# Kernel tuning notes

Hardware: AMD Instinct MI355X
Metric: run time of the kernel (lower is better)

Reference implementation:

```python
import jax, jax.numpy as jnp
import numpy as np

ALPHA = 0.5  # mixing weight between dot-product and wedge-norm terms


def setup_inputs() -> dict:
    key = jax.random.key(0)
    kq, kk, kv = jax.random.split(key, 3)
    B, L, H, E = 2, 2048, 8, 32
    queries = jax.random.normal(kq, (B, L, H, E), dtype=jnp.float32)
    keys = jax.random.normal(kk, (B, L, H, E), dtype=jnp.float32)
    values = jax.random.normal(kv, (B, L, H, E), dtype=jnp.float32)
    return {"queries": queries, "keys": keys, "values": values}


def reference(queries, keys, values):
    # queries: [B,L,H,E], keys: [B,S,H,E], values: [B,S,H,D]
    E = queries.shape[-1]
    scale = 1.0 / jnp.sqrt(jnp.asarray(E, dtype=queries.dtype))
    # dot product scores: [B,H,L,S]
    dot = jnp.einsum('blhe,bshe->bhls', queries, keys)
    # squared norms -> broadcastable [B,H,L,1] and [B,H,1,S]
    qn2 = jnp.sum(queries ** 2, axis=-1).transpose(0, 2, 1)[..., :, None]
    kn2 = jnp.sum(keys ** 2, axis=-1).transpose(0, 2, 1)[..., None, :]
    # wedge (Clifford) squared norm, clamped at 0
    wedge = jax.nn.relu(qn2 * kn2 - dot ** 2)
    scores = (ALPHA * dot - (1.0 - ALPHA) * wedge) * scale
    attn = jax.nn.softmax(scores, axis=-1)  # [B,H,L,S]
    # out: [B,L,H,D]
    out = jnp.einsum('bhls,bshd->blhd', attn, values)
    return out
```

## Files before the change

### kernel.cpp

```cpp
#include <hip/hip_runtime.h>
#include <hip/hip_bf16.h>
#include <math.h>


#define NB 2
#define NL 2048
#define NS 2048
#define NH 8
#define NBH 16
#define STRIPS 4
#define NT 16
#define CSC 0.12751742f
#define DEFER_THR 24.0f

#define WS_KN2_OFF 0u
#define WS_KHKL_OFF 131072u
#define WS_VT_OFF (131072u + 4194304u)
#define WS_PACC_OFF (131072u + 4194304u + 2097152u)
#define WS_PML_OFF (WS_PACC_OFF + 16777216u)
#define WS_NEED (WS_PML_OFF + 1048576u)

typedef float f32x4 __attribute__((ext_vector_type(4)));
typedef float f32x2 __attribute__((ext_vector_type(2)));
typedef short s16x8 __attribute__((ext_vector_type(8)));
typedef unsigned short u16;

__device__ inline unsigned pk2(float a, float b) {
    __hip_bfloat162 t = __float22bfloat162_rn(make_float2(a, b));
    union { __hip_bfloat162 h; unsigned u; } cv;
    cv.h = t;
    return cv.u;
}
template <int CTRL>
__device__ inline float dpp_add(float x) {
    return x + __int_as_float(__builtin_amdgcn_mov_dpp(__float_as_int(x), CTRL, 0xF, 0xF, false));
}
__device__ inline void dma16(const void* gp, void* lp) {
    __builtin_amdgcn_global_load_lds(
        (__attribute__((address_space(1))) void*)(void*)gp,
        (__attribute__((address_space(3))) void*)lp, 16, 0, 0);
}
__device__ inline void pl32(unsigned& a, unsigned& b) {
    asm("v_permlane32_swap_b32 %0, %1" : "+v"(a), "+v"(b));
}
__device__ inline void pl16(unsigned& a, unsigned& b) {
    asm("v_permlane16_swap_b32 %0, %1" : "+v"(a), "+v"(b));
}
__device__ inline int swzK(int row) { return (row ^ (row >> 2)) & 3; }
__device__ inline int swzV(int row) { return (row + (row >> 3)) & 7; }

__global__ __launch_bounds__(256) void ga_pre(const float* __restrict__ K,
                                              const float* __restrict__ V,
                                              float* __restrict__ kn2w,
                                              u16* __restrict__ khkl,
                                              u16* __restrict__ vtw) {
    __shared__ float Vf[64][36];
    const int T = threadIdx.x;
    const int bh = blockIdx.x >> 5, stile = blockIdx.x & 31;
    const int b = bh >> 3, h = bh & 7;
    const int s0 = stile * 64;
    const int sk = T >> 2, kc = T & 3;

    const float* kp = K + ((size_t)((b * NS + s0 + sk) * NH + h)) * 32 + kc * 8;
    float4 f0 = *(const float4*)kp, f1 = *(const float4*)(kp + 4);
    float kx[8] = {f0.x, f0.y, f0.z, f0.w, f1.x, f1.y, f1.z, f1.w};
    unsigned hh[4], ll[4];
    float kn2p = 0.f;
#pragma unroll
    for (int i = 0; i < 4; i++) {
        float x0 = kx[2 * i], x1 = kx[2 * i + 1];
        kn2p = fmaf(x0, x0, kn2p);
        kn2p = fmaf(x1, x1, kn2p);
        unsigned h01 = pk2(x0, x1);
        hh[i] = h01;
        float h0 = __uint_as_float(h01 << 16);
        float h1 = __uint_as_float(h01 & 0xffff0000u);
        ll[i] = pk2(x0 - h0, x1 - h1);
    }
    u16* kd = khkl + ((size_t)(bh * NS + s0 + sk)) * 64;
    const int swk = sk & 7;
    *(uint4*)(kd + ((kc ^ swk) * 8)) = make_uint4(hh[0], hh[1], hh[2], hh[3]);
    *(uint4*)(kd + (((4 + kc) ^ swk) * 8)) = make_uint4(ll[0], ll[1], ll[2], ll[3]);
    kn2p = dpp_add<0xB1>(kn2p);
    kn2p = dpp_add<0x4E>(kn2p);
    if (kc == 0) kn2w[bh * NS + s0 + sk] = kn2p;

    const float* vp = V + ((size_t)((b * NS + s0 + sk) * NH + h)) * 32 + kc * 8;
    float4 g0 = *(const float4*)vp, g1 = *(const float4*)(vp + 4);
    const int chv = kc ^ ((sk >> 3) & 3);
    *(float4*)&Vf[sk][chv * 8] = g0;
    *(float4*)&Vf[sk][chv * 8 + 4] = g1;
    __syncthreads();
    const int dr = T >> 3, c = T & 7;
    float vv[8];
#pragma unroll
    for (int i = 0; i < 8; i++)
        vv[i] = Vf[c * 8 + i][(((dr >> 3) ^ (c & 3)) << 3) + (dr & 7)];
    *(uint4*)(vtw + ((size_t)(bh * 32 + dr)) * NS + s0 + c * 8) =
        make_uint4(pk2(vv[0], vv[1]), pk2(vv[2], vv[3]), pk2(vv[4], vv[5]), pk2(vv[6], vv[7]));
}

__global__ __launch_bounds__(256, 3) void ga_wave(
    const float* __restrict__ Q, const float* __restrict__ kn2w,
    const u16* __restrict__ khkl, const u16* __restrict__ vtw,
    float* __restrict__ pacc, float* __restrict__ pml) {
    __shared__ u16 sK[4][2][32][64];
    __shared__ u16 sV[4][2][32][32];

    const int T = threadIdx.x;
    const int lane = T & 63, wave = T >> 6;
    const int g = lane >> 4, lc = lane & 15, g8 = g * 8;
    const int blk = blockIdx.x;
    const int qt = blk & 15, strip = (blk >> 4) & 3, bh = blk >> 6;
    const int b = bh >> 3, h = bh & 7;
    const int qwa = qt * 128 + wave * 16;
    const int qwb = qwa + 64;
    const int kb0 = strip * 512;

    s16x8 qha, qla, qhb, qlb;
    float qn2a, qn2b;
    {
        const float* qrow = Q + ((size_t)((b * NL + qwa + lc) * NH + h)) * 32 + g8;
        float4 qa = *(const float4*)qrow, qb = *(const float4*)(qrow + 4);
        float q8[8] = {qa.x, qa.y, qa.z, qa.w, qb.x, qb.y, qb.z, qb.w};
        union { unsigned u4[4]; s16x8 v; } qh_, ql_;
        float qn2 = 0.f;
#pragma unroll
        for (int i = 0; i < 4; i++) {
            float x0 = q8[2 * i], x1 = q8[2 * i + 1];
            qn2 = fmaf(x0, x0, qn2);
            qn2 = fmaf(x1, x1, qn2);
            unsigned h01 = pk2(x0, x1);
            qh_.u4[i] = h01;
            float h0 = __uint_as_float(h01 << 16);
            float h1 = __uint_as_float(h01 & 0xffff0000u);
            ql_.u4[i] = pk2(x0 - h0, x1 - h1);
        }
        qha = qh_.v; qla = ql_.v;
        qn2 += __shfl_xor(qn2, 16);
        qn2 += __shfl_xor(qn2, 32);
        qn2a = qn2;
    }
    {
        const float* qrow = Q + ((size_t)((b * NL + qwb + lc) * NH + h)) * 32 + g8;
        float4 qa = *(const float4*)qrow, qb = *(const float4*)(qrow + 4);
        float q8[8] = {qa.x, qa.y, qa.z, qa.w, qb.x, qb.y, qb.z, qb.w};
        union { unsigned u4[4]; s16x8 v; } qh_, ql_;
        float qn2 = 0.f;
#pragma unroll
        for (int i = 0; i < 4; i++) {
            float x0 = q8[2 * i], x1 = q8[2 * i + 1];
            qn2 = fmaf(x0, x0, qn2);
            qn2 = fmaf(x1, x1, qn2);
            unsigned h01 = pk2(x0, x1);
            qh_.u4[i] = h01;
            float h0 = __uint_as_float(h01 << 16);
            float h1 = __uint_as_float(h01 & 0xffff0000u);
            ql_.u4[i] = pk2(x0 - h0, x1 - h1);
        }
        qhb = qh_.v; qlb = ql_.v;
        qn2 += __shfl_xor(qn2, 16);
        qn2 += __shfl_xor(qn2, 32);
        qn2b = qn2;
    }

    const char* ksrc = (const char*)khkl + (size_t)(bh * NS + kb0) * 128 + lane * 16;
    const char* vsrc = (const char*)vtw +
        ((size_t)(bh * 32 + (lane >> 2)) * NS + kb0 + (lane & 3) * 8) * 2;
    const float* kn2b = kn2w + (size_t)bh * NS + kb0 + 4 * g;

    u16(*mK)[32][64] = sK[wave];
    u16(*mV)[32][32] = sV[wave];

    {
        dma16(ksrc, &mK[0][0][0]);
        dma16(ksrc + 1024, &mK[0][8][0]);
        dma16(ksrc + 2048, &mK[0][16][0]);
        dma16(ksrc + 3072, &mK[0][24][0]);
        dma16(vsrc, &mV[0][0][0]);
        dma16(vsrc + 16 * NS * 2, &mV[0][16][0]);
    }

    s16x8 ones;
#pragma unroll
    for (int i = 0; i < 8; i++) ones[i] = (short)0x3F80;

    f32x4 acc0a = {0.f, 0.f, 0.f, 0.f}, acc1a = {0.f, 0.f, 0.f, 0.f};
    f32x4 acc0b = {0.f, 0.f, 0.f, 0.f}, acc1b = {0.f, 0.f, 0.f, 0.f};
    f32x4 lacca = {0.f, 0.f, 0.f, 0.f}, laccb = {0.f, 0.f, 0.f, 0.f};
    float ma = -1e30f, mb = -1e30f;
    const f32x4 z = {0.f, 0.f, 0.f, 0.f};
    const int sw = lc & 7;

#pragma unroll 1
    for (int t = 0; t < NT; ++t) {
        asm volatile("s_waitcnt lgkmcnt(0)" ::: "memory");
        f32x4 kn20 = *(const f32x4*)(kn2b + t * 32);
        f32x4 kn21 = *(const f32x4*)(kn2b + t * 32 + 16);
        __builtin_amdgcn_sched_barrier(0);
        if (t + 1 < NT) {
            const char* k2 = ksrc + (size_t)(t + 1) * 4096;
            const char* v2 = vsrc + (size_t)(t + 1) * 64;
            const int nb = (t + 1) & 1;
            dma16(k2, &mK[nb][0][0]);
            dma16(k2 + 1024, &mK[nb][8][0]);
            dma16(k2 + 2048, &mK[nb][16][0]);
            dma16(k2 + 3072, &mK[nb][24][0]);
            dma16(v2, &mV[nb][0][0]);
            dma16(v2 + 16 * NS * 2, &mV[nb][16][0]);
            asm volatile("s_waitcnt vmcnt(6)" ::: "memory");
        } else {
            asm volatile("s_waitcnt vmcnt(0)" ::: "memory");
        }
        __builtin_amdgcn_sched_barrier(0);

        const int buf = t & 1;
        s16x8 kh0 = *(s16x8*)&mK[buf][lc][(g ^ sw) * 8];
        s16x8 kl0 = *(s16x8*)&mK[buf][lc][((4 + g) ^ sw) * 8];
        s16x8 kh1 = *(s16x8*)&mK[buf][16 + lc][(g ^ sw) * 8];
        s16x8 kl1 = *(s16x8*)&mK[buf][16 + lc][((4 + g) ^ sw) * 8];
        f32x4 da0, da1, db0, db1;
        {
            f32x4 dd = __builtin_amdgcn_mfma_f32_16x16x32_bf16(kl0, qha, z, 0, 0, 0);
            dd = __builtin_amdgcn_mfma_f32_16x16x32_bf16(kh0, qla, dd, 0, 0, 0);
            da0 = __builtin_amdgcn_mfma_f32_16x16x32_bf16(kh0, qha, dd, 0, 0, 0);
            dd = __builtin_amdgcn_mfma_f32_16x16x32_bf16(kl1, qha, z, 0, 0, 0);
            dd = __builtin_amdgcn_mfma_f32_16x16x32_bf16(kh1, qla, dd, 0, 0, 0);
            da1 = __builtin_amdgcn_mfma_f32_16x16x32_bf16(kh1, qha, dd, 0, 0, 0);
            dd = __builtin_amdgcn_mfma_f32_16x16x32_bf16(kl0, qhb, z, 0, 0, 0);
            dd = __builtin_amdgcn_mfma_f32_16x16x32_bf16(kh0, qlb, dd, 0, 0, 0);
            db0 = __builtin_amdgcn_mfma_f32_16x16x32_bf16(kh0, qhb, dd, 0, 0, 0);
            dd = __builtin_amdgcn_mfma_f32_16x16x32_bf16(kl1, qhb, z, 0, 0, 0);
            dd = __builtin_amdgcn_mfma_f32_16x16x32_bf16(kh1, qlb, dd, 0, 0, 0);
            db1 = __builtin_amdgcn_mfma_f32_16x16x32_bf16(kh1, qhb, dd, 0, 0, 0);
        }
        s16x8 vlo = *(s16x8*)&mV[buf][lc][g8];
        s16x8 vhi = *(s16x8*)&mV[buf][16 + lc][g8];

        float sca[2][4], scb[2][4];
        {
            const f32x2 qa2 = {qn2a, qn2a}, qb2 = {qn2b, qn2b};
            f32x4 kn2m[2] = {kn20, kn21};
            f32x4 dam[2] = {da0, da1}, dbm[2] = {db0, db1};
#pragma unroll
            for (int st = 0; st < 2; st++) {
                f32x2 kk0 = {kn2m[st][0], kn2m[st][1]}, kk1 = {kn2m[st][2], kn2m[st][3]};
                f32x2 dd0 = {dam[st][0], dam[st][1]}, dd1 = {dam[st][2], dam[st][3]};
                f32x2 e0 = dd0 - qa2 * kk0;
                f32x2 e1 = dd1 - qa2 * kk1;
                f32x2 t0 = dd0 * dd0 + e0;
                f32x2 t1 = dd1 * dd1 + e1;
                sca[st][0] = fminf(dam[st][0], t0[0]);
                sca[st][1] = fminf(dam[st][1], t0[1]);
                sca[st][2] = fminf(dam[st][2], t1[0]);
                sca[st][3] = fminf(dam[st][3], t1[1]);
                f32x2 ee0 = {dbm[st][0], dbm[st][1]}, ee1 = {dbm[st][2], dbm[st][3]};
                f32x2 f0 = ee0 - qb2 * kk0;
                f32x2 f1 = ee1 - qb2 * kk1;
                f32x2 u0 = ee0 * ee0 + f0;
                f32x2 u1 = ee1 * ee1 + f1;
                scb[st][0] = fminf(dbm[st][0], u0[0]);
                scb[st][1] = fminf(dbm[st][1], u0[1]);
                scb[st][2] = fminf(dbm[st][2], u1[0]);
                scb[st][3] = fminf(dbm[st][3], u1[1]);
            }
        }

        float tma = fmaxf(fmaxf(fmaxf(sca[0][0], sca[0][1]), fmaxf(sca[0][2], sca[0][3])),
                          fmaxf(fmaxf(sca[1][0], sca[1][1]), fmaxf(sca[1][2], sca[1][3])));
        float tmb = fmaxf(fmaxf(fmaxf(scb[0][0], scb[0][1]), fmaxf(scb[0][2], scb[0][3])),
                          fmaxf(fmaxf(scb[1][0], scb[1][1]), fmaxf(scb[1][2], scb[1][3])));
        if (!__all((tma <= ma + DEFER_THR) && (tmb <= mb + DEFER_THR))) {
            tma = fmaxf(tma, __shfl_xor(tma, 16));
            tma = fmaxf(tma, __shfl_xor(tma, 32));
            tmb = fmaxf(tmb, __shfl_xor(tmb, 16));
            tmb = fmaxf(tmb, __shfl_xor(tmb, 32));
            const float nma = fmaxf(ma, tma), nmb = fmaxf(mb, tmb);
            const float ala = __builtin_amdgcn_exp2f((ma - nma) * CSC);
            const float alb = __builtin_amdgcn_exp2f((mb - nmb) * CSC);
            ma = nma; mb = nmb;
            acc0a *= ala; acc1a *= ala; lacca *= ala;
            acc0b *= alb; acc1b *= alb; laccb *= alb;
        }
        const float negmaC = -ma * CSC, negmbC = -mb * CSC;
        const f32x2 cscv = {CSC, CSC};
        const f32x2 nmav = {negmaC, negmaC}, nmbv = {negmbC, negmbC};
        float pa[2][4], pb[2][4];
#pragma unroll
        for (int st = 0; st < 2; st++) {
            f32x2 s0 = {sca[st][0], sca[st][1]}, s1 = {sca[st][2], sca[st][3]};
            f32x2 e0 = s0 * cscv + nmav;
            f32x2 e1 = s1 * cscv + nmav;
            pa[st][0] = __builtin_amdgcn_exp2f(e0[0]);
            pa[st][1] = __builtin_amdgcn_exp2f(e0[1]);
            pa[st][2] = __builtin_amdgcn_exp2f(e1[0]);
            pa[st][3] = __builtin_amdgcn_exp2f(e1[1]);
            f32x2 u0 = {scb[st][0], scb[st][1]}, u1 = {scb[st][2], scb[st][3]};
            f32x2 f0 = u0 * cscv + nmbv;
            f32x2 f1 = u1 * cscv + nmbv;
            pb[st][0] = __builtin_amdgcn_exp2f(f0[0]);
            pb[st][1] = __builtin_amdgcn_exp2f(f0[1]);
            pb[st][2] = __builtin_amdgcn_exp2f(f1[0]);
            pb[st][3] = __builtin_amdgcn_exp2f(f1[1]);
        }

        {
            unsigned w00 = pk2(pa[0][0], pa[0][1]), w01 = pk2(pa[0][2], pa[0][3]);
            unsigned w10 = pk2(pa[1][0], pa[1][1]), w11 = pk2(pa[1][2], pa[1][3]);
            pl32(w00, w10); pl32(w01, w11);
            pl16(w00, w10); pl16(w01, w11);
            union { uint4 u; s16x8 v; } P;
            P.u = make_uint4(w00, w01, w10, w11);
            acc0a = __builtin_amdgcn_mfma_f32_16x16x32_bf16(vlo, P.v, acc0a, 0, 0, 0);
            acc1a = __builtin_amdgcn_mfma_f32_16x16x32_bf16(vhi, P.v, acc1a, 0, 0, 0);
            lacca = __builtin_amdgcn_mfma_f32_16x16x32_bf16(ones, P.v, lacca, 0, 0, 0);
        }
        {
            unsigned w00 = pk2(pb[0][0], pb[0][1]), w01 = pk2(pb[0][2], pb[0][3]);
            unsigned w10 = pk2(pb[1][0], pb[1][1]), w11 = pk2(pb[1][2], pb[1][3]);
            pl32(w00, w10); pl32(w01, w11);
            pl16(w00, w10); pl16(w01, w11);
            union { uint4 u; s16x8 v; } P;
            P.u = make_uint4(w00, w01, w10, w11);
            acc0b = __builtin_amdgcn_mfma_f32_16x16x32_bf16(vlo, P.v, acc0b, 0, 0, 0);
            acc1b = __builtin_amdgcn_mfma_f32_16x16x32_bf16(vhi, P.v, acc1b, 0, 0, 0);
            laccb = __builtin_amdgcn_mfma_f32_16x16x32_bf16(ones, P.v, laccb, 0, 0, 0);
        }
    }

    float* paa = pacc + (((size_t)bh * STRIPS + strip) * NL + (qwa + lc)) * 32;
    *(f32x4*)(paa + 4 * g) = acc0a;
    *(f32x4*)(paa + 16 + 4 * g) = acc1a;
    float* pab = pacc + (((size_t)bh * STRIPS + strip) * NL + (qwb + lc)) * 32;
    *(f32x4*)(pab + 4 * g) = acc0b;
    *(f32x4*)(pab + 16 + 4 * g) = acc1b;
    if (g == 0) {
        *(float2*)(pml + (((size_t)bh * STRIPS + strip) * NL + (qwa + lc)) * 2) =
            make_float2(ma, lacca[0]);
        *(float2*)(pml + (((size_t)bh * STRIPS + strip) * NL + (qwb + lc)) * 2) =
            make_float2(mb, laccb[0]);
    }
}

__global__ __launch_bounds__(256) void ga_combine(const float* __restrict__ pacc,
                                                  const float* __restrict__ pml,
                                                  float* __restrict__ O) {
    const int tid = blockIdx.x * 256 + threadIdx.x;
    const int dq = tid & 7, q = (tid >> 3) & 2047, bh = tid >> 14;
    const int b = bh >> 3, h = bh & 7;
    float m[4], l[4];
#pragma unroll
    for (int s = 0; s < 4; s++) {
        float2 t = *(const float2*)(pml + (((size_t)bh * STRIPS + s) * NL + q) * 2);
        m[s] = t.x;
        l[s] = t.y;
    }
    float mf = fmaxf(fmaxf(m[0], m[1]), fmaxf(m[2], m[3]));
    float w[4], L = 0.f;
#pragma unroll
    for (int s = 0; s < 4; s++) {
        w[s] = __builtin_amdgcn_exp2f((m[s] - mf) * CSC);
        L = fmaf(l[s], w[s], L);
    }
    const float inv = 1.f / L;
    float4 o = make_float4(0.f, 0.f, 0.f, 0.f);
#pragma unroll
    for (int s = 0; s < 4; s++) {
        const float* pa = pacc + (((size_t)bh * STRIPS + s) * NL + q) * 32 + dq * 4;
        float4 a = *(const float4*)pa;
        o.x = fmaf(a.x, w[s], o.x);
        o.y = fmaf(a.y, w[s], o.y);
        o.z = fmaf(a.z, w[s], o.z);
        o.w = fmaf(a.w, w[s], o.w);
    }
    o.x *= inv; o.y *= inv; o.z *= inv; o.w *= inv;
    *(float4*)(O + (((size_t)(b * NL + q)) * NH + h) * 32 + dq * 4) = o;
}

__global__ __launch_bounds__(512, 4) void ga_fallback(
    const float* __restrict__ Q, const float* __restrict__ K,
    const float* __restrict__ V, float* __restrict__ O) {
    __shared__ union {
        struct {
            u16 Kh[2][64][32];
            u16 Kl[2][64][32];
            u16 Vt[2][32][64];
            float kn2[2][64];
        } s;
        struct { float acc[8][32][17]; float m[8][16]; float l[8][16]; } c;
    } u;
    __shared__ u16 sP[8][16][64];

    const int T = threadIdx.x;
    const int lane = T & 63, wave = T >> 6;
    const int g = lane >> 4, lc = lane & 15, g8 = g * 8;
    const int half = wave >> 2;
    const int qt = blockIdx.x & 31;
    const int bh = blockIdx.x >> 5;
    const int b = bh >> 3, h = bh & 7;
    const int qw = qt * 64 + (wave & 3) * 16;

    const float* qrow = Q + ((size_t)((b * NL + qw + lc) * NH + h)) * 32 + g8;
    float4 qa = *(const float4*)qrow, qb = *(const float4*)(qrow + 4);
    float q8[8] = {qa.x, qa.y, qa.z, qa.w, qb.x, qb.y, qb.z, qb.w};
    union { unsigned u4[4]; s16x8 v; } qh_, ql_;
    float qn2 = 0.f;
#pragma unroll
    for (int i = 0; i < 4; i++) {
        float x0 = q8[2 * i], x1 = q8[2 * i + 1];
        qn2 = fmaf(x0, x0, qn2);
        qn2 = fmaf(x1, x1, qn2);
        unsigned h01 = pk2(x0, x1);
        qh_.u4[i] = h01;
        float h0 = __uint_as_float(h01 << 16);
        float h1 = __uint_as_float(h01 & 0xffff0000u);
        ql_.u4[i] = pk2(x0 - h0, x1 - h1);
    }
    const s16x8 qh = qh_.v, ql = ql_.v;
    qn2 += __shfl_xor(qn2, 16);
    qn2 += __shfl_xor(qn2, 32);

    const int Tl = T & 255;
    const int sk = Tl >> 2, kc = Tl & 3;
    const int dv = Tl & 31, vc = Tl >> 5;
    const float* kbase = K + ((size_t)(b * NS * NH) + h) * 32;
    const float* vbase = V + ((size_t)(b * NS * NH) + h) * 32;
    const int kphys = (kc ^ swzK(sk)) * 8;
    const int vphys = (vc ^ swzV(dv)) * 8;

    int s0 = half * 1024;
    float4 ka = *(const float4*)(kbase + (size_t)(s0 + sk) * 256 + kc * 8);
    float4 kb = *(const float4*)(kbase + (size_t)(s0 + sk) * 256 + kc * 8 + 4);
    float vr[8];
#pragma unroll
    for (int i = 0; i < 8; i++) vr[i] = vbase[(size_t)(s0 + 8 * vc + i) * 256 + dv];

    f32x4 acc0 = {0.f, 0.f, 0.f, 0.f}, acc1 = {0.f, 0.f, 0.f, 0.f};
    float m = -INFINITY, l = 0.f;

    for (int t = 0; t < 16; ++t) {
        {
            float kx[8] = {ka.x, ka.y, ka.z, ka.w, kb.x, kb.y, kb.z, kb.w};
            unsigned hh[4], ll[4];
            float kn2p = 0.f;
#pragma unroll
            for (int i = 0; i < 4; i++) {
                float x0 = kx[2 * i], x1 = kx[2 * i + 1];
                kn2p = fmaf(x0, x0, kn2p);
                kn2p = fmaf(x1, x1, kn2p);
                unsigned h01 = pk2(x0, x1);
                hh[i] = h01;
                float h0 = __uint_as_float(h01 << 16);
                float h1 = __uint_as_float(h01 & 0xffff0000u);
                ll[i] = pk2(x0 - h0, x1 - h1);
            }
            *(uint4*)&u.s.Kh[half][sk][kphys] = make_uint4(hh[0], hh[1], hh[2], hh[3]);
            *(uint4*)&u.s.Kl[half][sk][kphys] = make_uint4(ll[0], ll[1], ll[2], ll[3]);
            kn2p = dpp_add<0xB1>(kn2p);
            kn2p = dpp_add<0x4E>(kn2p);
            if (kc == 0) u.s.kn2[half][sk] = kn2p;
            *(uint4*)&u.s.Vt[half][dv][vphys] =
                make_uint4(pk2(vr[0], vr[1]), pk2(vr[2], vr[3]),
                           pk2(vr[4], vr[5]), pk2(vr[6], vr[7]));
        }
        const int tn = (t + 1 < 16) ? t + 1 : t;
        const int sn = half * 1024 + tn * 64;
        ka = *(const float4*)(kbase + (size_t)(sn + sk) * 256 + kc * 8);
        kb = *(const float4*)(kbase + (size_t)(sn + sk) * 256 + kc * 8 + 4);
#pragma unroll
        for (int i = 0; i < 8; i++) vr[i] = vbase[(size_t)(sn + 8 * vc + i) * 256 + dv];

        __syncthreads();

        f32x4 d[4], kn2v[4];
        const f32x4 z = {0.f, 0.f, 0.f, 0.f};
        const int skr = swzK(lc);
#pragma unroll
        for (int st = 0; st < 4; st++) {
            kn2v[st] = *(f32x4*)&u.s.kn2[half][16 * st + 4 * g];
            s16x8 kh = *(s16x8*)&u.s.Kh[half][16 * st + lc][(g ^ skr) * 8];
            s16x8 kl = *(s16x8*)&u.s.Kl[half][16 * st + lc][(g ^ skr) * 8];
            f32x4 dd = __builtin_amdgcn_mfma_f32_16x16x32_bf16(kl, qh, z, 0, 0, 0);
            dd = __builtin_amdgcn_mfma_f32_16x16x32_bf16(kh, ql, dd, 0, 0, 0);
            dd = __builtin_amdgcn_mfma_f32_16x16x32_bf16(kh, qh, dd, 0, 0, 0);
            d[st] = dd;
        }

        float sc[4][4];
#pragma unroll
        for (int st = 0; st < 4; st++)
#pragma unroll
            for (int r = 0; r < 4; r++) {
                float dd = d[st][r];
                float w = fmaxf(fmaf(-dd, dd, qn2 * kn2v[st][r]), 0.f);
                sc[st][r] = (dd - w) * CSC;
            }

        float x0 = fmaxf(fmaxf(sc[0][0], sc[0][1]), fmaxf(sc[0][2], sc[0][3]));
        float x1 = fmaxf(fmaxf(sc[1][0], sc[1][1]), fmaxf(sc[1][2], sc[1][3]));
        float x2 = fmaxf(fmaxf(sc[2][0], sc[2][1]), fmaxf(sc[2][2], sc[2][3]));
        float x3 = fmaxf(fmaxf(sc[3][0], sc[3][1]), fmaxf(sc[3][2], sc[3][3]));
        float tm = fmaxf(fmaxf(x0, x1), fmaxf(x2, x3));
        tm = fmaxf(tm, __shfl_xor(tm, 16));
        tm = fmaxf(tm, __shfl_xor(tm, 32));
        const float nm = fmaxf(m, tm);
        const float al = __builtin_amdgcn_exp2f(m - nm);
        m = nm;
        float p[4][4], ls = 0.f;
#pragma unroll
        for (int st = 0; st < 4; st++)
#pragma unroll
            for (int r = 0; r < 4; r++) {
                p[st][r] = __builtin_amdgcn_exp2f(sc[st][r] - nm);
                ls += p[st][r];
            }
        l = fmaf(l, al, ls);
        acc0 *= al;
        acc1 *= al;

#pragma unroll
        for (int st = 0; st < 4; st++) {
            const int off = ((2 * st + (g >> 1)) ^ (lc & 7)) * 8 + (g & 1) * 4;
            *(uint2*)&sP[wave][lc][off] =
                make_uint2(pk2(p[st][0], p[st][1]), pk2(p[st][2], p[st][3]));
        }
        __builtin_amdgcn_s_waitcnt(0xC07F);

        const int svl = swzV(lc), svh = swzV(lc + 16), spl = lc & 7;
        s16x8 va00 = *(s16x8*)&u.s.Vt[half][lc][(g ^ svl) * 8];
        s16x8 va01 = *(s16x8*)&u.s.Vt[half][lc][((4 + g) ^ svl) * 8];
        s16x8 va10 = *(s16x8*)&u.s.Vt[half][lc + 16][(g ^ svh) * 8];
        s16x8 va11 = *(s16x8*)&u.s.Vt[half][lc + 16][((4 + g) ^ svh) * 8];
        s16x8 pb0 = *(s16x8*)&sP[wave][lc][(g ^ spl) * 8];
        s16x8 pb1 = *(s16x8*)&sP[wave][lc][((4 + g) ^ spl) * 8];
        acc0 = __builtin_amdgcn_mfma_f32_16x16x32_bf16(va00, pb0, acc0, 0, 0, 0);
        acc0 = __builtin_amdgcn_mfma_f32_16x16x32_bf16(va01, pb1, acc0, 0, 0, 0);
        acc1 = __builtin_amdgcn_mfma_f32_16x16x32_bf16(va10, pb0, acc1, 0, 0, 0);
        acc1 = __builtin_amdgcn_mfma_f32_16x16x32_bf16(va11, pb1, acc1, 0, 0, 0);

        __syncthreads();
    }

    l += __shfl_xor(l, 16);
    l += __shfl_xor(l, 32);
#pragma unroll
    for (int r = 0; r < 4; r++) {
        u.c.acc[wave][4 * g + r][lc] = acc0[r];
        u.c.acc[wave][16 + 4 * g + r][lc] = acc1[r];
    }
    if (lane < 16) {
        u.c.m[wave][lc] = m;
        u.c.l[wave][lc] = l;
    }
    __syncthreads();

    const int q = T >> 3, dq = (T & 7) * 4, qr = q & 15;
    const int w0 = q >> 4, w1 = w0 + 4;
    float m0 = u.c.m[w0][qr], m1 = u.c.m[w1][qr];
    float l0 = u.c.l[w0][qr], l1 = u.c.l[w1][qr];
    float mf = fmaxf(m0, m1);
    float e0 = __builtin_amdgcn_exp2f(m0 - mf);
    float e1 = __builtin_amdgcn_exp2f(m1 - mf);
    float inv = 1.f / fmaf(l1, e1, l0 * e0);
    e0 *= inv;
    e1 *= inv;
    float4 o;
    o.x = u.c.acc[w0][dq + 0][qr] * e0 + u.c.acc[w1][dq + 0][qr] * e1;
    o.y = u.c.acc[w0][dq + 1][qr] * e0 + u.c.acc[w1][dq + 1][qr] * e1;
    o.z = u.c.acc[w0][dq + 2][qr] * e0 + u.c.acc[w1][dq + 2][qr] * e1;
    o.w = u.c.acc[w0][dq + 3][qr] * e0 + u.c.acc[w1][dq + 3][qr] * e1;
    *(float4*)(O + ((size_t)((b * NL + qt * 64 + q) * NH + h)) * 32 + dq) = o;
}

extern "C" void kernel_launch(void* const* d_in, const int* in_sizes, int n_in,
                              void* d_out, int out_size, void* d_ws, size_t ws_size,
                              hipStream_t stream) {
    const float* Q = (const float*)d_in[0];
    const float* K = (const float*)d_in[1];
    const float* V = (const float*)d_in[2];
    float* O = (float*)d_out;

    if (ws_size >= (size_t)WS_NEED) {
        float* kn2w = (float*)((char*)d_ws + WS_KN2_OFF);
        u16* khkl = (u16*)((char*)d_ws + WS_KHKL_OFF);
        u16* vtw = (u16*)((char*)d_ws + WS_VT_OFF);
        float* pacc = (float*)((char*)d_ws + WS_PACC_OFF);
        float* pml = (float*)((char*)d_ws + WS_PML_OFF);
        ga_pre<<<NBH * 32, 256, 0, stream>>>(K, V, kn2w, khkl, vtw);
        ga_wave<<<NBH * 16 * STRIPS, 256, 0, stream>>>(Q, kn2w, khkl, vtw, pacc, pml);
        ga_combine<<<(NBH * NL * 8) / 256, 256, 0, stream>>>(pacc, pml, O);
    } else {
        ga_fallback<<<NBH * 32, 512, 0, stream>>>(Q, K, V, O);
    }
}
```

Measured before the change: 106.8 us.

## Replace per-wave LDS DMA staging with register double-buffered global loads

The main attention kernel stops staging K/V tiles through per-wave LDS buffers filled by global_load_lds DMA. Each lane now loads its MFMA operands straight from global memory into registers, double-buffered across two tile sets (A/B) so the next tile's loads overlap the current tile's compute. The K swizzle in the preprocessing kernel is removed to match the direct loads. The block index mapping is also reordered so consecutive blocks share a query tile across (bh, strip) groups. This frees LDS and drops the LDS round-trip, at the cost of more VGPRs and of relying on L2/cache for the reuse of K/V across waves.

```diff
diff --git a/kernel.cpp b/kernel.cpp
--- a/kernel.cpp
+++ b/kernel.cpp
@@ -34,11 +34,6 @@
 template <int CTRL>
 __device__ inline float dpp_add(float x) {
     return x + __int_as_float(__builtin_amdgcn_mov_dpp(__float_as_int(x), CTRL, 0xF, 0xF, false));
-}
-__device__ inline void dma16(const void* gp, void* lp) {
-    __builtin_amdgcn_global_load_lds(
-        (__attribute__((address_space(1))) void*)(void*)gp,
-        (__attribute__((address_space(3))) void*)lp, 16, 0, 0);
 }
 __device__ inline void pl32(unsigned& a, unsigned& b) {
     asm("v_permlane32_swap_b32 %0, %1" : "+v"(a), "+v"(b));
@@ -78,9 +73,8 @@
         ll[i] = pk2(x0 - h0, x1 - h1);
     }
     u16* kd = khkl + ((size_t)(bh * NS + s0 + sk)) * 64;
-    const int swk = sk & 7;
-    *(uint4*)(kd + ((kc ^ swk) * 8)) = make_uint4(hh[0], hh[1], hh[2], hh[3]);
-    *(uint4*)(kd + (((4 + kc) ^ swk) * 8)) = make_uint4(ll[0], ll[1], ll[2], ll[3]);
+    *(uint4*)(kd + kc * 8) = make_uint4(hh[0], hh[1], hh[2], hh[3]);
+    *(uint4*)(kd + (4 + kc) * 8) = make_uint4(ll[0], ll[1], ll[2], ll[3]);
     kn2p = dpp_add<0xB1>(kn2p);
     kn2p = dpp_add<0x4E>(kn2p);
     if (kc == 0) kn2w[bh * NS + s0 + sk] = kn2p;
@@ -100,18 +94,16 @@
         make_uint4(pk2(vv[0], vv[1]), pk2(vv[2], vv[3]), pk2(vv[4], vv[5]), pk2(vv[6], vv[7]));
 }
 
-__global__ __launch_bounds__(256, 3) void ga_wave(
+__global__ __launch_bounds__(256, 3) void ga_rpipe(
     const float* __restrict__ Q, const float* __restrict__ kn2w,
     const u16* __restrict__ khkl, const u16* __restrict__ vtw,
     float* __restrict__ pacc, float* __restrict__ pml) {
-    __shared__ u16 sK[4][2][32][64];
-    __shared__ u16 sV[4][2][32][32];
-
     const int T = threadIdx.x;
     const int lane = T & 63, wave = T >> 6;
     const int g = lane >> 4, lc = lane & 15, g8 = g * 8;
     const int blk = blockIdx.x;
-    const int qt = blk & 15, strip = (blk >> 4) & 3, bh = blk >> 6;
+    const int qt = blk >> 6, grp = blk & 63;
+    const int bh = grp >> 2, strip = grp & 3;
     const int b = bh >> 3, h = bh & 7;
     const int qwa = qt * 128 + wave * 16;
     const int qwb = qwa + 64;
@@ -164,22 +156,9 @@
         qn2b = qn2;
     }
 
-    const char* ksrc = (const char*)khkl + (size_t)(bh * NS + kb0) * 128 + lane * 16;
-    const char* vsrc = (const char*)vtw +
-        ((size_t)(bh * 32 + (lane >> 2)) * NS + kb0 + (lane & 3) * 8) * 2;
-    const float* kn2b = kn2w + (size_t)bh * NS + kb0 + 4 * g;
-
-    u16(*mK)[32][64] = sK[wave];
-    u16(*mV)[32][32] = sV[wave];
-
-    {
-        dma16(ksrc, &mK[0][0][0]);
-        dma16(ksrc + 1024, &mK[0][8][0]);
-        dma16(ksrc + 2048, &mK[0][16][0]);
-        dma16(ksrc + 3072, &mK[0][24][0]);
-        dma16(vsrc, &mV[0][0][0]);
-        dma16(vsrc + 16 * NS * 2, &mV[0][16][0]);
-    }
+    const u16* kimg = khkl + ((size_t)(bh * NS + kb0) + lc) * 64 + g8;
+    const u16* vimg = vtw + ((size_t)(bh * 32 + lc)) * NS + kb0 + g8;
+    const float* knb = kn2w + (size_t)bh * NS + kb0 + 4 * g;
 
     s16x8 ones;
 #pragma unroll
@@ -190,35 +169,29 @@
     f32x4 lacca = {0.f, 0.f, 0.f, 0.f}, laccb = {0.f, 0.f, 0.f, 0.f};
     float ma = -1e30f, mb = -1e30f;
     const f32x4 z = {0.f, 0.f, 0.f, 0.f};
-    const int sw = lc & 7;
-
-#pragma unroll 1
-    for (int t = 0; t < NT; ++t) {
-        asm volatile("s_waitcnt lgkmcnt(0)" ::: "memory");
-        f32x4 kn20 = *(const f32x4*)(kn2b + t * 32);
-        f32x4 kn21 = *(const f32x4*)(kn2b + t * 32 + 16);
-        __builtin_amdgcn_sched_barrier(0);
-        if (t + 1 < NT) {
-            const char* k2 = ksrc + (size_t)(t + 1) * 4096;
-            const char* v2 = vsrc + (size_t)(t + 1) * 64;
-            const int nb = (t + 1) & 1;
-            dma16(k2, &mK[nb][0][0]);
-            dma16(k2 + 1024, &mK[nb][8][0]);
-            dma16(k2 + 2048, &mK[nb][16][0]);
-            dma16(k2 + 3072, &mK[nb][24][0]);
-            dma16(v2, &mV[nb][0][0]);
-            dma16(v2 + 16 * NS * 2, &mV[nb][16][0]);
-            asm volatile("s_waitcnt vmcnt(6)" ::: "memory");
-        } else {
-            asm volatile("s_waitcnt vmcnt(0)" ::: "memory");
-        }
-        __builtin_amdgcn_sched_barrier(0);
-
-        const int buf = t & 1;
-        s16x8 kh0 = *(s16x8*)&mK[buf][lc][(g ^ sw) * 8];
-        s16x8 kl0 = *(s16x8*)&mK[buf][lc][((4 + g) ^ sw) * 8];
-        s16x8 kh1 = *(s16x8*)&mK[buf][16 + lc][(g ^ sw) * 8];
-        s16x8 kl1 = *(s16x8*)&mK[buf][16 + lc][((4 + g) ^ sw) * 8];
+
+    s16x8 Akh0, Akl0, Akh1, Akl1, Av0, Av1;
+    f32x4 Akn0, Akn1;
+    s16x8 Bkh0, Bkl0, Bkh1, Bkl1, Bv0, Bv1;
+    f32x4 Bkn0, Bkn1;
+
+#define LOAD_TILE(S, tt)                                                       \
+    do {                                                                       \
+        const u16* kr = kimg + (size_t)(tt) * (32 * 64);                       \
+        S##kh0 = *(const s16x8*)(kr);                                          \
+        S##kl0 = *(const s16x8*)(kr + 32);                                     \
+        S##kh1 = *(const s16x8*)(kr + 16 * 64);                                \
+        S##kl1 = *(const s16x8*)(kr + 16 * 64 + 32);                           \
+        const u16* vr = vimg + (size_t)(tt) * 32;                              \
+        S##v0 = *(const s16x8*)(vr);                                           \
+        S##v1 = *(const s16x8*)(vr + 16 * NS);                                 \
+        const float* kn = knb + (size_t)(tt) * 32;                             \
+        S##kn0 = *(const f32x4*)(kn);                                          \
+        S##kn1 = *(const f32x4*)(kn + 16);                                     \
+    } while (0)
+
+    auto compute = [&](s16x8 kh0, s16x8 kl0, s16x8 kh1, s16x8 kl1,
+                       s16x8 vlo, s16x8 vhi, f32x4 kn20, f32x4 kn21) {
         f32x4 da0, da1, db0, db1;
         {
             f32x4 dd = __builtin_amdgcn_mfma_f32_16x16x32_bf16(kl0, qha, z, 0, 0, 0);
@@ -234,8 +207,6 @@
             dd = __builtin_amdgcn_mfma_f32_16x16x32_bf16(kh1, qlb, dd, 0, 0, 0);
             db1 = __builtin_amdgcn_mfma_f32_16x16x32_bf16(kh1, qhb, dd, 0, 0, 0);
         }
-        s16x8 vlo = *(s16x8*)&mV[buf][lc][g8];
-        s16x8 vhi = *(s16x8*)&mV[buf][16 + lc][g8];
 
         float sca[2][4], scb[2][4];
         {
@@ -326,7 +297,21 @@
             acc1b = __builtin_amdgcn_mfma_f32_16x16x32_bf16(vhi, P.v, acc1b, 0, 0, 0);
             laccb = __builtin_amdgcn_mfma_f32_16x16x32_bf16(ones, P.v, laccb, 0, 0, 0);
         }
-    }
+    };
+
+    LOAD_TILE(A, 0);
+#pragma unroll 1
+    for (int t = 0; t < NT; t += 2) {
+        LOAD_TILE(B, t + 1);
+        __builtin_amdgcn_sched_barrier(0);
+        compute(Akh0, Akl0, Akh1, Akl1, Av0, Av1, Akn0, Akn1);
+        if (t + 2 < NT) {
+            LOAD_TILE(A, t + 2);
+        }
+        __builtin_amdgcn_sched_barrier(0);
+        compute(Bkh0, Bkl0, Bkh1, Bkl1, Bv0, Bv1, Bkn0, Bkn1);
+    }
+#undef LOAD_TILE
 
     float* paa = pacc + (((size_t)bh * STRIPS + strip) * NL + (qwa + lc)) * 32;
     *(f32x4*)(paa + 4 * g) = acc0a;
@@ -587,7 +572,7 @@
         float* pacc = (float*)((char*)d_ws + WS_PACC_OFF);
         float* pml = (float*)((char*)d_ws + WS_PML_OFF);
         ga_pre<<<NBH * 32, 256, 0, stream>>>(K, V, kn2w, khkl, vtw);
-        ga_wave<<<NBH * 16 * STRIPS, 256, 0, stream>>>(Q, kn2w, khkl, vtw, pacc, pml);
+        ga_rpipe<<<NBH * 16 * STRIPS, 256, 0, stream>>>(Q, kn2w, khkl, vtw, pacc, pml);
         ga_combine<<<(NBH * NL * 8) / 256, 256, 0, stream>>>(pacc, pml, O);
     } else {
         ga_fallback<<<NBH * 32, 512, 0, stream>>>(Q, K, V, O);
```

Measured after the change: 120.2 us. 1.13x slower.
